# Kernel tuning notes

Measured on AMD Instinct MI355X. Metric: run time of the kernel, lower is better.

The kernel has to match this reference:

```python
import jax, jax.numpy as jnp
import numpy as np
from jax import lax

GAMMA = 0.01
BIG = 1e8  # stand-in for +inf on DP borders (keeps grads finite/zero)


def _pairwise_sq_dists(x, y):
    # x: [N,1] (target), y: [N,1] (pred) -> D[i,j] = (x_i - y_j)^2
    xn = jnp.sum(x * x, axis=1)  # [N]
    yn = jnp.sum(y * y, axis=1)  # [N]
    d = xn[:, None] + yn[None, :] - 2.0 * (x @ y.T)
    return jnp.maximum(d, 0.0)


def _soft_dtw(D, gamma):
    # Soft-DTW DP via wavefront scan over the 2N-1 anti-diagonals.
    # R[i,j] = D[i,j] + softmin_gamma(R[i-1,j-1], R[i-1,j], R[i,j-1]),
    # with virtual R[-1,-1] = 0 and +inf borders.
    N = D.shape[0]
    ii = jnp.arange(N)

    def shift(r):  # r[i] -> r[i-1], BIG at i=0
        return jnp.concatenate([jnp.full((1,), BIG, r.dtype), r[:-1]])

    def step(carry, k):
        r1, r2 = carry  # diagonals k-1 and k-2, indexed by row i
        jj = k - ii
        valid = (jj >= 0) & (jj < N)
        d = D[ii, jnp.clip(jj, 0, N - 1)]
        a = shift(r2)                                   # R[i-1, j-1]
        a = jnp.where((k == 0) & (ii == 0), 0.0, a)     # virtual origin
        b = shift(r1)                                   # R[i-1, j]
        c = jnp.where(jj >= 1, r1, BIG)                 # R[i, j-1]
        vals = jnp.stack([a, b, c])                     # [3, N]
        m = jnp.min(vals, axis=0)
        softmin = m - gamma * jnp.log(jnp.sum(jnp.exp(-(vals - m) / gamma), axis=0))
        r_new = jnp.where(valid, d + softmin, BIG)
        return (r_new, r1), None

    init = jnp.full((N,), BIG, D.dtype)
    (r_last, _), _ = lax.scan(step, (init, init), jnp.arange(2 * N - 1))
    return r_last[N - 1]  # R[N-1, N-1], batch size 1 -> mean == value


def setup_inputs() -> dict:
    key = jax.random.key(0)
    k1, k2 = jax.random.split(key)
    pred = jax.random.normal(k1, (4096, 1), dtype=jnp.float32)
    target = jax.random.normal(k2, (4096, 1), dtype=jnp.float32)
    return {"pred": pred, "target": target}


def reference(pred, target):
    # DILATELoss.forward returns loss_shape (the soft-DTW value);
    # the temporal path term is computed in the original but discarded.
    D = _pairwise_sq_dists(target.reshape(-1, 1), pred.reshape(-1, 1))
    return _soft_dtw(D, GAMMA)
```

## Files before the change

### kernel.cpp

```cpp
#include <hip/hip_runtime.h>

#define NN    4096
#define BIGF  1e8f
#define SQK2f 12.0112245225638540f
#define BIGK  1.4426950408889634e10f
#define IK2f  0.00693147180559945309f
#define NBLK  32
#define SCH   16
#define NCI   260
#define OUTS  4158
#define SENTU 0xFFFFFFFFu

__global__ __launch_bounds__(1024) void dilate_sdtw(const float* __restrict__ pred,
                                                    const float* __restrict__ target,
                                                    float* __restrict__ out) {
    __shared__ float t_s[NN];
    __shared__ float p_s[NN];
    __shared__ float bufA[NN];
    __shared__ float bufB[NN];
    __shared__ float bufC[NN];
    const int tid = threadIdx.x;
    for (int i = tid; i < NN; i += 1024) {
        t_s[i] = target[i]; p_s[i] = pred[i];
        bufA[i] = BIGF; bufB[i] = BIGF; bufC[i] = BIGF;
    }
    __syncthreads();
    float* r2 = bufA; float* r1 = bufB; float* rn = bufC;
    for (int k = 0; k < 2 * NN - 1; ++k) {
        int ilo = k - (NN - 1); if (ilo < 0) ilo = 0;
        int ihi = (k < NN - 1) ? k : (NN - 1);
        for (int i = ilo + tid; i <= ihi; i += 1024) {
            const int j = k - i;
            float diff = t_s[i] - p_s[j];
            float d = diff * diff;
            float a = (i >= 1 && j >= 1) ? r2[i - 1] : ((k == 0) ? 0.0f : BIGF);
            float b = (i >= 1) ? r1[i - 1] : BIGF;
            float c = (j >= 1) ? r1[i] : BIGF;
            float m = fminf(a, fminf(b, c));
            float s = __expf((m - a) * 100.0f) + __expf((m - b) * 100.0f) + __expf((m - c) * 100.0f);
            rn[i] = d + m - 0.01f * __logf(s);
        }
        __syncthreads();
        float* tmp = r2; r2 = r1; r1 = rn; rn = tmp;
    }
    if (tid == 0) out[0] = r1[NN - 1];
}


__device__ __forceinline__ float softmin3s(float a, float b, float c) {
    float m = fminf(a, fminf(b, c));
    float e = __builtin_amdgcn_exp2f(m - a)
            + __builtin_amdgcn_exp2f(m - b)
            + __builtin_amdgcn_exp2f(m - c);
    return m - __builtin_amdgcn_logf(e);
}

__device__ __forceinline__ float nbr1(float v, bool bsel) {
    int iv = __float_as_int(v);
    float a = __int_as_float(__builtin_amdgcn_update_dpp(iv, iv, 0x111, 0xF, 0xF, false));
    float b = __int_as_float(__builtin_amdgcn_update_dpp(iv, iv, 0x142, 0xF, 0xF, false));
    return bsel ? b : a;
}

__device__ __forceinline__ void bput(float* p, float v) {
    __hip_atomic_store((unsigned int*)p, __float_as_uint(v),
                       __ATOMIC_RELAXED, __HIP_MEMORY_SCOPE_AGENT);
}
__device__ __forceinline__ unsigned int bgetu(const float* p) {
    return __hip_atomic_load((const unsigned int*)p,
                             __ATOMIC_RELAXED, __HIP_MEMORY_SCOPE_AGENT);
}

__device__ __forceinline__ void uissue(const float* src, float* dst) {
#pragma unroll
    for (int q = 0; q < SCH; ++q) dst[q] = __uint_as_float(bgetu(src + q));
}
__device__ __forceinline__ bool uvalid(const float* dst) {
    bool ok = true;
#pragma unroll
    for (int q = 0; q < SCH; ++q) ok &= (__float_as_uint(dst[q]) != SENTU);
    return ok;
}
__device__ __forceinline__ void upoll(const float* src, float* dst) {
    for (;;) {
        uissue(src, dst);
        if (uvalid(dst)) return;
        __builtin_amdgcn_s_sleep(1);
    }
}

__device__ __forceinline__ void pload(const float* p_s, int base, float* dst) {
#pragma unroll
    for (int q = 0; q < SCH; ++q) {
        int idx = base + q;
        idx = idx < 0 ? 0 : (idx > NN - 1 ? NN - 1 : idx);
        dst[q] = p_s[idx];
    }
}

template<bool TOP, bool BOT, bool EDGE>
__device__ __forceinline__ void chunk16(
    int cs, int lane, bool l0, bool bsel, float t0, float t1,
    float& v0, float& v1, float& u1, float& u2, float upl,
    float4& acc, const float* upc, const float* pc,
    float* __restrict__ bnd_my, float* __restrict__ outp)
{
#pragma unroll
    for (int u = 0; u < SCH; ++u) {
        const int s = cs + u;
        const int j = s - lane;
        float a, b;
        if (TOP) {
            a = l0 ? ((s == 0) ? 0.0f : BIGK) : u2;
            b = l0 ? BIGK : u1;
        } else {
            float upj  = upc[u];
            float upjm = (u == 0) ? upl : upc[u - 1];
            a = l0 ? upjm : u2;
            b = l0 ? upj  : u1;
        }
        float pj = pc[u];
        float d0 = t0 - pj;
        float val0 = fmaf(d0, d0, softmin3s(a, b, v0));
        float d1 = t1 - pj;
        float val1 = fmaf(d1, d1, softmin3s(v0, val0, v1));
        if (EDGE) {
            bool vj = (unsigned)j < (unsigned)NN;
            val0 = vj ? val0 : BIGK;
            val1 = vj ? val1 : BIGK;
        }
        if (!BOT) {
            switch ((u + 1) & 3) {
                case 0: acc.x = val1; break;
                case 1: acc.y = val1; break;
                case 2: acc.z = val1; break;
                case 3: acc.w = val1; break;
            }
            if ((u & 3) == 2) {
                int base = j - 3;
                if (lane == 63 && (!EDGE || (unsigned)base <= (unsigned)(NN - 4))) {
                    bput(bnd_my + base + 0, acc.x);
                    bput(bnd_my + base + 1, acc.y);
                    bput(bnd_my + base + 2, acc.z);
                    bput(bnd_my + base + 3, acc.w);
                }
            }
        } else if (EDGE) {
            if (lane == 63 && s == OUTS) outp[0] = val1 * IK2f;
        }
        v0 = val0; v1 = val1;
        u2 = u1;
        u1 = nbr1(val1, bsel);
    }
}

template<bool TOP, bool BOT>
__device__ __forceinline__ void chunk_iter(
    int ci, int lane, bool l0, bool bsel, float t0, float t1,
    float& v0, float& v1, float& u1, float& u2, float& upl,
    float4& acc,
    float* upC, float* upN, float* pcC, float* pcN,
    const float* p_s, const float* __restrict__ bnd_up, float* __restrict__ bnd_my,
    float* __restrict__ outp)
{
    const int cs = SCH * ci;
    if (!TOP && cs < NN) {
        if (!uvalid(upC)) upoll(bnd_up + cs, upC);
        if (cs + SCH < NN) uissue(bnd_up + cs + SCH, upN);
    }
    if (ci + 1 < NCI) pload(p_s, cs + SCH - lane, pcN);

    const bool edge = (ci < 4) || (ci >= 256);
    if (edge) chunk16<TOP, BOT, true >(cs, lane, l0, bsel, t0, t1, v0, v1, u1, u2,
                                       upl, acc, upC, pcC, bnd_my, outp);
    else      chunk16<TOP, BOT, false>(cs, lane, l0, bsel, t0, t1, v0, v1, u1, u2,
                                       upl, acc, upC, pcC, bnd_my, outp);
    if (!TOP) upl = upC[SCH - 1];
}

template<bool TOP, bool BOT>
__device__ void stripe(int b, int lane, const float* __restrict__ target,
                       const float* p_s, float* bnd, float* outp)
{
    const float t0 = target[128 * b + 2 * lane]     * SQK2f;
    const float t1 = target[128 * b + 2 * lane + 1] * SQK2f;
    float* bnd_my = bnd + (size_t)b * NN;
    const float* bnd_up = bnd + (size_t)(b - 1) * NN;
    const bool l0 = (lane == 0);
    const bool bsel = (lane != 0) && ((lane & 15) == 0);

    float v0 = BIGK, v1 = BIGK, u1 = BIGK, u2 = BIGK, upl = BIGK;
    float4 acc = {BIGK, BIGK, BIGK, BIGK};
    float upA[SCH], upB[SCH];
    float pcA[SCH], pcB[SCH];

    pload(p_s, -lane, pcA);
    if (!TOP) uissue(bnd_up, upA);

    for (int cp = 0; cp < NCI / 2; ++cp) {
        chunk_iter<TOP, BOT>(2 * cp,     lane, l0, bsel, t0, t1, v0, v1, u1, u2, upl, acc,
                             upA, upB, pcA, pcB, p_s, bnd_up, bnd_my, outp);
        chunk_iter<TOP, BOT>(2 * cp + 1, lane, l0, bsel, t0, t1, v0, v1, u1, u2, upl, acc,
                             upB, upA, pcB, pcA, p_s, bnd_up, bnd_my, outp);
    }
}

__global__ __launch_bounds__(64, 1) void sdtw_pipe16(const float* __restrict__ pred,
                                                     const float* __restrict__ target,
                                                     float* __restrict__ out,
                                                     float* __restrict__ bnd)
{
    __shared__ float p_s[NN];
    const int lane = threadIdx.x;
    const int bid = blockIdx.x;
    const int b = (bid & 7) * 4 + (bid >> 3);
    for (int i = lane; i < NN; i += 64) p_s[i] = pred[i] * SQK2f;
    __syncthreads();
    if (b == 0)                stripe<true , false>(b, lane, target, p_s, bnd, out);
    else if (b == NBLK - 1)    stripe<false, true >(b, lane, target, p_s, bnd, out);
    else                       stripe<false, false>(b, lane, target, p_s, bnd, out);
}

extern "C" void kernel_launch(void* const* d_in, const int* in_sizes, int n_in,
                              void* d_out, int out_size, void* d_ws, size_t ws_size,
                              hipStream_t stream) {
    const float* pred   = (const float*)d_in[0];
    const float* target = (const float*)d_in[1];
    float* out = (float*)d_out;

    const size_t need = (size_t)NBLK * NN * sizeof(float);
    if (ws_size >= need) {
        float* bnd = (float*)d_ws;
        hipMemsetAsync(d_ws, 0xFF, need, stream);
        sdtw_pipe16<<<dim3(NBLK), dim3(64), 0, stream>>>(pred, target, out, bnd);
    } else {
        dilate_sdtw<<<dim3(1), dim3(1024), 0, stream>>>(pred, target, out);
    }
}
```

Measured before the change: 857.6 us.

## Split the DP into 64 one-row-per-lane stripes instead of 32 two-row stripes

Adds a new wavefront kernel in which each lane owns a single DP row, so 64 blocks of 64 lanes each cover one 64-row stripe. Previously 32 blocks each computed two rows per lane, with two chained softmins per step. Halving the serial per-lane work per anti-diagonal step is meant to shorten the critical path. In exchange there are twice as many pipeline stages, each adding its own startup lag and cross-block boundary handoff through global memory. The old two-row kernel is kept as a fallback for smaller workspaces.

```diff
diff --git a/kernel.cpp b/kernel.cpp
--- a/kernel.cpp
+++ b/kernel.cpp
@@ -5,11 +5,13 @@
 #define SQK2f 12.0112245225638540f
 #define BIGK  1.4426950408889634e10f
 #define IK2f  0.00693147180559945309f
-#define NBLK  32
 #define SCH   16
 #define NCI   260
 #define OUTS  4158
 #define SENTU 0xFFFFFFFFu
+
+#define NB2   32
+#define NB1   64
 
 __global__ __launch_bounds__(1024) void dilate_sdtw(const float* __restrict__ pred,
                                                     const float* __restrict__ target,
@@ -98,10 +100,11 @@
     }
 }
 
+
 template<bool TOP, bool BOT, bool EDGE>
-__device__ __forceinline__ void chunk16(
-    int cs, int lane, bool l0, bool bsel, float t0, float t1,
-    float& v0, float& v1, float& u1, float& u2, float upl,
+__device__ __forceinline__ void chunkR1(
+    int cs, int lane, bool l0, bool bsel, float t,
+    float& v, float& u1, float& u2, float upl,
     float4& acc, const float* upc, const float* pc,
     float* __restrict__ bnd_my, float* __restrict__ outp)
 {
@@ -119,6 +122,111 @@
             a = l0 ? upjm : u2;
             b = l0 ? upj  : u1;
         }
+        float d = t - pc[u];
+        float val = fmaf(d, d, softmin3s(a, b, v));
+        if (EDGE) val = ((unsigned)j < (unsigned)NN) ? val : BIGK;
+        if (!BOT) {
+            switch ((u + 1) & 3) {
+                case 0: acc.x = val; break;
+                case 1: acc.y = val; break;
+                case 2: acc.z = val; break;
+                case 3: acc.w = val; break;
+            }
+            if ((u & 3) == 2) {
+                const int base = j - 3;
+                if (lane == 63 && (!EDGE || (unsigned)base <= (unsigned)(NN - 4))) {
+                    bput(bnd_my + base + 0, acc.x);
+                    bput(bnd_my + base + 1, acc.y);
+                    bput(bnd_my + base + 2, acc.z);
+                    bput(bnd_my + base + 3, acc.w);
+                }
+            }
+        } else if (EDGE) {
+            if (lane == 63 && s == OUTS) outp[0] = val * IK2f;
+        }
+        v = val;
+        u2 = u1;
+        u1 = nbr1(val, bsel);
+    }
+}
+
+template<bool TOP, bool BOT>
+__device__ void stripeR1(int b, int lane, const float* __restrict__ target,
+                         const float* p_s, float* bnd, float* outp)
+{
+    const float t = target[64 * b + lane] * SQK2f;
+    float* bnd_my = bnd + (size_t)b * NN;
+    const float* bnd_up = bnd + (size_t)(b - 1) * NN;
+    const bool l0 = (lane == 0);
+    const bool bsel = (lane != 0) && ((lane & 15) == 0);
+
+    float v = BIGK, u1 = BIGK, u2 = BIGK, upl = BIGK;
+    float4 acc = {BIGK, BIGK, BIGK, BIGK};
+    float upA[SCH], upB[SCH];
+    float pcA[SCH], pcB[SCH];
+
+    pload(p_s, -lane, pcA);
+    if (!TOP) uissue(bnd_up, upA);
+
+    for (int cp = 0; cp < NCI / 2; ++cp) {
+        for (int half = 0; half < 2; ++half) {
+            const int ci = 2 * cp + half;
+            float* upC = half ? upB : upA;
+            float* upN = half ? upA : upB;
+            float* pcC = half ? pcB : pcA;
+            float* pcN = half ? pcA : pcB;
+            const int cs = SCH * ci;
+            if (!TOP && cs < NN) {
+                if (!uvalid(upC)) upoll(bnd_up + cs, upC);
+                if (cs + SCH < NN) uissue(bnd_up + cs + SCH, upN);
+            }
+            if (ci + 1 < NCI) pload(p_s, cs + SCH - lane, pcN);
+            const bool edge = (ci < 4) || (ci >= 256);
+            if (edge) chunkR1<TOP, BOT, true >(cs, lane, l0, bsel, t, v, u1, u2, upl, acc, upC, pcC, bnd_my, outp);
+            else      chunkR1<TOP, BOT, false>(cs, lane, l0, bsel, t, v, u1, u2, upl, acc, upC, pcC, bnd_my, outp);
+            if (!TOP && cs < NN) upl = upC[SCH - 1];
+        }
+    }
+}
+
+__global__ __launch_bounds__(64, 1) void sdtw_r1(const float* __restrict__ pred,
+                                                 const float* __restrict__ target,
+                                                 float* __restrict__ out,
+                                                 float* __restrict__ bnd)
+{
+    __shared__ float p_s[NN];
+    const int lane = threadIdx.x;
+    const int bid = blockIdx.x;
+    const int b = (bid & 7) * 8 + (bid >> 3);
+    for (int i = lane; i < NN; i += 64) p_s[i] = pred[i] * SQK2f;
+    __syncthreads();
+    if (b == 0)              stripeR1<true , false>(b, lane, target, p_s, bnd, out);
+    else if (b == NB1 - 1)   stripeR1<false, true >(b, lane, target, p_s, bnd, out);
+    else                     stripeR1<false, false>(b, lane, target, p_s, bnd, out);
+}
+
+
+template<bool TOP, bool BOT, bool EDGE>
+__device__ __forceinline__ void chunkR2(
+    int cs, int lane, bool l0, bool bsel, float t0, float t1,
+    float& v0, float& v1, float& u1, float& u2, float upl,
+    float4& acc, const float* upc, const float* pc,
+    float* __restrict__ bnd_my, float* __restrict__ outp)
+{
+#pragma unroll
+    for (int u = 0; u < SCH; ++u) {
+        const int s = cs + u;
+        const int j = s - lane;
+        float a, b;
+        if (TOP) {
+            a = l0 ? ((s == 0) ? 0.0f : BIGK) : u2;
+            b = l0 ? BIGK : u1;
+        } else {
+            float upj  = upc[u];
+            float upjm = (u == 0) ? upl : upc[u - 1];
+            a = l0 ? upjm : u2;
+            b = l0 ? upj  : u1;
+        }
         float pj = pc[u];
         float d0 = t0 - pj;
         float val0 = fmaf(d0, d0, softmin3s(a, b, v0));
@@ -155,32 +263,8 @@
 }
 
 template<bool TOP, bool BOT>
-__device__ __forceinline__ void chunk_iter(
-    int ci, int lane, bool l0, bool bsel, float t0, float t1,
-    float& v0, float& v1, float& u1, float& u2, float& upl,
-    float4& acc,
-    float* upC, float* upN, float* pcC, float* pcN,
-    const float* p_s, const float* __restrict__ bnd_up, float* __restrict__ bnd_my,
-    float* __restrict__ outp)
-{
-    const int cs = SCH * ci;
-    if (!TOP && cs < NN) {
-        if (!uvalid(upC)) upoll(bnd_up + cs, upC);
-        if (cs + SCH < NN) uissue(bnd_up + cs + SCH, upN);
-    }
-    if (ci + 1 < NCI) pload(p_s, cs + SCH - lane, pcN);
-
-    const bool edge = (ci < 4) || (ci >= 256);
-    if (edge) chunk16<TOP, BOT, true >(cs, lane, l0, bsel, t0, t1, v0, v1, u1, u2,
-                                       upl, acc, upC, pcC, bnd_my, outp);
-    else      chunk16<TOP, BOT, false>(cs, lane, l0, bsel, t0, t1, v0, v1, u1, u2,
-                                       upl, acc, upC, pcC, bnd_my, outp);
-    if (!TOP) upl = upC[SCH - 1];
-}
-
-template<bool TOP, bool BOT>
-__device__ void stripe(int b, int lane, const float* __restrict__ target,
-                       const float* p_s, float* bnd, float* outp)
+__device__ void stripeR2(int b, int lane, const float* __restrict__ target,
+                         const float* p_s, float* bnd, float* outp)
 {
     const float t0 = target[128 * b + 2 * lane]     * SQK2f;
     const float t1 = target[128 * b + 2 * lane + 1] * SQK2f;
@@ -198,17 +282,30 @@
     if (!TOP) uissue(bnd_up, upA);
 
     for (int cp = 0; cp < NCI / 2; ++cp) {
-        chunk_iter<TOP, BOT>(2 * cp,     lane, l0, bsel, t0, t1, v0, v1, u1, u2, upl, acc,
-                             upA, upB, pcA, pcB, p_s, bnd_up, bnd_my, outp);
-        chunk_iter<TOP, BOT>(2 * cp + 1, lane, l0, bsel, t0, t1, v0, v1, u1, u2, upl, acc,
-                             upB, upA, pcB, pcA, p_s, bnd_up, bnd_my, outp);
-    }
-}
-
-__global__ __launch_bounds__(64, 1) void sdtw_pipe16(const float* __restrict__ pred,
-                                                     const float* __restrict__ target,
-                                                     float* __restrict__ out,
-                                                     float* __restrict__ bnd)
+        for (int half = 0; half < 2; ++half) {
+            const int ci = 2 * cp + half;
+            float* upC = half ? upB : upA;
+            float* upN = half ? upA : upB;
+            float* pcC = half ? pcB : pcA;
+            float* pcN = half ? pcA : pcB;
+            const int cs = SCH * ci;
+            if (!TOP && cs < NN) {
+                if (!uvalid(upC)) upoll(bnd_up + cs, upC);
+                if (cs + SCH < NN) uissue(bnd_up + cs + SCH, upN);
+            }
+            if (ci + 1 < NCI) pload(p_s, cs + SCH - lane, pcN);
+            const bool edge = (ci < 4) || (ci >= 256);
+            if (edge) chunkR2<TOP, BOT, true >(cs, lane, l0, bsel, t0, t1, v0, v1, u1, u2, upl, acc, upC, pcC, bnd_my, outp);
+            else      chunkR2<TOP, BOT, false>(cs, lane, l0, bsel, t0, t1, v0, v1, u1, u2, upl, acc, upC, pcC, bnd_my, outp);
+            if (!TOP && cs < NN) upl = upC[SCH - 1];
+        }
+    }
+}
+
+__global__ __launch_bounds__(64, 1) void sdtw_r2(const float* __restrict__ pred,
+                                                 const float* __restrict__ target,
+                                                 float* __restrict__ out,
+                                                 float* __restrict__ bnd)
 {
     __shared__ float p_s[NN];
     const int lane = threadIdx.x;
@@ -216,9 +313,9 @@
     const int b = (bid & 7) * 4 + (bid >> 3);
     for (int i = lane; i < NN; i += 64) p_s[i] = pred[i] * SQK2f;
     __syncthreads();
-    if (b == 0)                stripe<true , false>(b, lane, target, p_s, bnd, out);
-    else if (b == NBLK - 1)    stripe<false, true >(b, lane, target, p_s, bnd, out);
-    else                       stripe<false, false>(b, lane, target, p_s, bnd, out);
+    if (b == 0)              stripeR2<true , false>(b, lane, target, p_s, bnd, out);
+    else if (b == NB2 - 1)   stripeR2<false, true >(b, lane, target, p_s, bnd, out);
+    else                     stripeR2<false, false>(b, lane, target, p_s, bnd, out);
 }
 
 extern "C" void kernel_launch(void* const* d_in, const int* in_sizes, int n_in,
@@ -228,11 +325,16 @@
     const float* target = (const float*)d_in[1];
     float* out = (float*)d_out;
 
-    const size_t need = (size_t)NBLK * NN * sizeof(float);
-    if (ws_size >= need) {
+    const size_t need1 = (size_t)(NB1 - 1) * NN * sizeof(float);
+    const size_t need2 = (size_t)NB2 * NN * sizeof(float);
+    if (ws_size >= need1) {
         float* bnd = (float*)d_ws;
-        hipMemsetAsync(d_ws, 0xFF, need, stream);
-        sdtw_pipe16<<<dim3(NBLK), dim3(64), 0, stream>>>(pred, target, out, bnd);
+        hipMemsetAsync(d_ws, 0xFF, need1, stream);
+        sdtw_r1<<<dim3(NB1), dim3(64), 0, stream>>>(pred, target, out, bnd);
+    } else if (ws_size >= need2) {
+        float* bnd = (float*)d_ws;
+        hipMemsetAsync(d_ws, 0xFF, need2, stream);
+        sdtw_r2<<<dim3(NB2), dim3(64), 0, stream>>>(pred, target, out, bnd);
     } else {
         dilate_sdtw<<<dim3(1), dim3(1024), 0, stream>>>(pred, target, out);
     }
```

Result: slower. 2.260 ms (+163.6%).
